# Performance work log

Measured on AMD Instinct MI355X. Metric: run time of the kernel, lower is better.

Reference implementation:

```python
import jax, jax.numpy as jnp
import numpy as np

D_MODEL = 768
NUM_HEADS = 12
D_K = D_MODEL // NUM_HEADS
WINDOW = 16
SPARSITY = 0.8
NEG = -1e9


def _pos_encoding(seq_len, d_model, dtype):
    pos = jnp.arange(seq_len, dtype=jnp.float32)[:, None]
    div = jnp.exp(jnp.arange(0, d_model, 2, dtype=jnp.float32) * (-np.log(10000.0) / d_model))
    pe = jnp.zeros((seq_len, d_model), dtype=jnp.float32)
    pe = pe.at[:, 0::2].set(jnp.sin(pos * div))
    pe = pe.at[:, 1::2].set(jnp.cos(pos * div))
    return pe.astype(dtype)


def _layernorm(x, gamma, beta, eps=1e-5):
    mu = jnp.mean(x, axis=-1, keepdims=True)
    var = jnp.mean(jnp.square(x - mu), axis=-1, keepdims=True)
    return (x - mu) * jax.lax.rsqrt(var + eps) * gamma + beta


def _split_heads(x):  # [B,S,D] -> [B,H,S,dk]
    b, s, _ = x.shape
    return x.reshape(b, s, NUM_HEADS, D_K).transpose(0, 2, 1, 3)


def _attn(q, k, v, mask):  # mask broadcastable to [B,H,S,S], bool
    scores = jnp.einsum('bhqd,bhkd->bhqk', q, k) / jnp.sqrt(jnp.asarray(D_K, q.dtype))
    scores = jnp.where(mask, scores, jnp.asarray(NEG, q.dtype))
    w = jax.nn.softmax(scores, axis=-1)
    out = jnp.einsum('bhqk,bhkd->bhqd', w, v)
    b, h, s, d = out.shape
    return out.transpose(0, 2, 1, 3).reshape(b, s, h * d)


def setup_inputs() -> dict:
    key = jax.random.key(0)
    ks = jax.random.split(key, 16)
    d = D_MODEL
    sc = 1.0 / np.sqrt(d)
    inp = {
        'x': jax.random.normal(ks[0], (2, 2048, d), jnp.float32),
        'wgq': jax.random.normal(ks[1], (d, d), jnp.float32) * sc,
        'wgk': jax.random.normal(ks[2], (d, d), jnp.float32) * sc,
        'wgv': jax.random.normal(ks[3], (d, d), jnp.float32) * sc,
        'wlq': jax.random.normal(ks[4], (d, d), jnp.float32) * sc,
        'wlk': jax.random.normal(ks[5], (d, d), jnp.float32) * sc,
        'wlv': jax.random.normal(ks[6], (d, d), jnp.float32) * sc,
        'wtq': jax.random.normal(ks[7], (d, d), jnp.float32) * sc,
        'wtk': jax.random.normal(ks[8], (d, d), jnp.float32) * sc,
        'wtv': jax.random.normal(ks[9], (d, d), jnp.float32) * sc,
        'w_out': jax.random.normal(ks[10], (3 * d, d), jnp.float32) * (1.0 / np.sqrt(3 * d)),
        'b_out': jnp.zeros((d,), jnp.float32),
        'w_gate': jax.random.normal(ks[11], (d, 3), jnp.float32) * sc,
        'b_gate': jnp.zeros((3,), jnp.float32),
        'w_sparse': jax.random.normal(ks[12], (d, 1), jnp.float32) * sc,
        'b_sparse': jnp.zeros((1,), jnp.float32),
        'g_gamma': jnp.ones((d,), jnp.float32), 'g_beta': jnp.zeros((d,), jnp.float32),
        'l_gamma': jnp.ones((d,), jnp.float32), 'l_beta': jnp.zeros((d,), jnp.float32),
        't_gamma': jnp.ones((d,), jnp.float32), 't_beta': jnp.zeros((d,), jnp.float32),
    }
    return inp


def reference(x, wgq, wgk, wgv, wlq, wlk, wlv, wtq, wtk, wtv,
              w_out, b_out, w_gate, b_gate, w_sparse, b_sparse,
              g_gamma, g_beta, l_gamma, l_beta, t_gamma, t_beta):
    b, s, d = x.shape
    # positional encoding branch input (dropout is identity at eval)
    x_pos = x + _pos_encoding(s, d, x.dtype)[None]

    # focus gate over mean-pooled tokens -> [B,3]
    fw = jax.nn.softmax(x.mean(axis=1) @ w_gate + b_gate, axis=-1)
    gw, lw, tw = fw[:, 0, None, None], fw[:, 1, None, None], fw[:, 2, None, None]

    # sparse (global) mask: keep top-k important columns per batch
    importance = (x @ w_sparse + b_sparse)[..., 0]  # [B,S]
    k = max(1, int((1.0 - SPARSITY) * s))
    _, topk_idx = jax.lax.top_k(importance, k)
    sparse = jnp.zeros((b, s), bool).at[jnp.arange(b)[:, None], topk_idx].set(True)
    sparse_mask = sparse[:, None, None, :]  # [B,1,1,S]

    idx = jnp.arange(s)
    rel = idx[None, :] - idx[:, None]
    half = WINDOW // 2
    local_mask = ((rel >= -half) & (rel <= half))[None, None]  # [1,1,S,S]

    stride = max(1, s // 8)
    temporal_cols = (idx % stride) == 0
    temporal_mask = jnp.broadcast_to(temporal_cols[None, :], (s, s))[None, None]

    # global branch
    g = _attn(_split_heads(x @ wgq), _split_heads(x @ wgk), _split_heads(x @ wgv), sparse_mask)
    g = _layernorm(g, g_gamma, g_beta)
    # local branch
    l = _attn(_split_heads(x @ wlq), _split_heads(x @ wlk), _split_heads(x @ wlv), local_mask)
    l = _layernorm(l, l_gamma, l_beta)
    # temporal branch (uses pos-encoded input)
    t = _attn(_split_heads(x_pos @ wtq), _split_heads(x_pos @ wtk), _split_heads(x_pos @ wtv), temporal_mask)
    t = _layernorm(t, t_gamma, t_beta)

    combined = jnp.concatenate([g * gw, l * lw, t * tw], axis=-1)
    return combined @ w_out + b_out
```

## Files before the change

### kernel.cpp

```cpp
#include <hip/hip_runtime.h>
#include <cstdint>

constexpr int BB   = 2;
constexpr int SS   = 2048;
constexpr int DD   = 768;
constexpr int HH   = 12;
constexpr int NTOK = BB * SS;
constexpr int KSEL = 409;
constexpr int KPAD = 448;
constexpr int NKT  = 7;

typedef __bf16 bf16x8 __attribute__((ext_vector_type(8)));
typedef float  f32x4  __attribute__((ext_vector_type(4)));

__device__ __forceinline__ float b2f(unsigned short u) {
  return __uint_as_float(((unsigned)u) << 16);
}
__device__ __forceinline__ unsigned short f2b(float f) {
  unsigned u = __float_as_uint(f);
  u += 0x7fffu + ((u >> 16) & 1u);
  return (unsigned short)(u >> 16);
}
__device__ __forceinline__ unsigned long long shfl_xor_u64(unsigned long long v, int m) {
  unsigned lo = (unsigned)v, hi = (unsigned)(v >> 32);
  lo = __shfl_xor(lo, m, 64);
  hi = __shfl_xor(hi, m, 64);
  return ((unsigned long long)hi << 32) | lo;
}

__device__ __forceinline__ void gload_lds16(const void* gsrc, void* ldst) {
  __builtin_amdgcn_global_load_lds(
      (__attribute__((address_space(1))) void*)(gsrc),
      (__attribute__((address_space(3))) void*)(ldst), 16, 0, 0);
}

__global__ __launch_bounds__(256) void prep_imp(const float* __restrict__ x,
                                                const float* __restrict__ wsp,
                                                const float* __restrict__ bsp,
                                                unsigned short* __restrict__ xb,
                                                unsigned short* __restrict__ xpb,
                                                float* __restrict__ imp) {
  int srow = blockIdx.x;
  int tid = threadIdx.x;
  const float* xr0 = x + (long)srow * DD;
  const float* xr1 = x + (long)(SS + srow) * DD;
  float acc0 = 0.f, acc1 = 0.f;
#pragma unroll
  for (int k = 0; k < 3; ++k) {
    int c = tid + k * 256;
    int j2 = c & ~1;
    float freq = __expf((float)j2 * -0.011992630692677323f);
    float ang = (float)srow * freq;
    float pe = (c & 1) ? cosf(ang) : sinf(ang);
    float w = wsp[c];
    float x0 = xr0[c], x1 = xr1[c];
    xb[(long)srow * DD + c]        = f2b(x0);
    xb[(long)(SS + srow) * DD + c] = f2b(x1);
    xpb[(long)srow * DD + c]        = f2b(x0 + pe);
    xpb[(long)(SS + srow) * DD + c] = f2b(x1 + pe);
    acc0 += x0 * w;
    acc1 += x1 * w;
  }
#pragma unroll
  for (int m = 1; m < 64; m <<= 1) {
    acc0 += __shfl_xor(acc0, m, 64);
    acc1 += __shfl_xor(acc1, m, 64);
  }
  __shared__ float red[8];
  int wv = tid >> 6, lane = tid & 63;
  if (lane == 0) { red[wv] = acc0; red[4 + wv] = acc1; }
  __syncthreads();
  if (tid == 0) {
    imp[srow]      = red[0] + red[1] + red[2] + red[3] + bsp[0];
    imp[SS + srow] = red[4] + red[5] + red[6] + red[7] + bsp[0];
  }
}

__global__ void transpose_all(const float* w0, const float* w1, const float* w2,
                              const float* w3, const float* w4, const float* w5,
                              const float* w6, const float* w7, const float* w8,
                              const float* w9,
                              unsigned short* WTx4, unsigned short* WTkv,
                              unsigned short* WTqt, unsigned short* WTtkv,
                              unsigned short* WTo) {
  __shared__ float tile[32][33];
  int id = blockIdx.x;
  int z, bx, by;
  if (id < 5184) { z = id / 576; int rem = id % 576; by = rem / 24; bx = rem % 24; }
  else           { z = 9; int rem = id - 5184; by = rem / 24; bx = rem % 24; }
  const float* srcs[10] = {w0, w1, w2, w3, w4, w5, w6, w7, w8, w9};
  const float* src = srcs[z];
  unsigned short* dst;
  int R = DD;
  switch (z) {
    case 0: dst = WTx4;                       break;
    case 1: dst = WTkv;                       break;
    case 2: dst = WTkv + (long)DD * DD;       break;
    case 3: dst = WTx4 + (long)DD * DD;       break;
    case 4: dst = WTx4 + (long)2 * DD * DD;   break;
    case 5: dst = WTx4 + (long)3 * DD * DD;   break;
    case 6: dst = WTqt;                       break;
    case 7: dst = WTtkv;                      break;
    case 8: dst = WTtkv + (long)DD * DD;      break;
    default: dst = WTo; R = 2304;             break;
  }
  int r0 = by * 32;
  int c0 = bx * 32;
  int tx = threadIdx.x, ty = threadIdx.y;
  for (int i = ty; i < 32; i += 8) tile[i][tx] = src[(long)(r0 + i) * DD + c0 + tx];
  __syncthreads();
  for (int i = ty; i < 32; i += 8) dst[(long)(c0 + i) * R + r0 + tx] = f2b(tile[tx][i]);
}

__global__ __launch_bounds__(1024) void topk_kernel(const float* __restrict__ imp,
                                                    int* __restrict__ sel) {
  __shared__ unsigned long long keys[SS];
  int b = blockIdx.x, tid = threadIdx.x;
  for (int i = tid; i < SS; i += 1024) {
    float v = imp[b * SS + i];
    unsigned u = __float_as_uint(v);
    u = (u & 0x80000000u) ? ~u : (u | 0x80000000u);
    unsigned du = ~u;
    keys[i] = ((unsigned long long)du << 32) | (unsigned)i;
  }
  __syncthreads();
  for (int k = 2; k <= SS; k <<= 1) {
    for (int j = k >> 1; j >= 64; j >>= 1) {
      for (int i = tid; i < SS; i += 1024) {
        int p = i ^ j;
        if (p > i) {
          unsigned long long a = keys[i], bb = keys[p];
          bool up = ((i & k) == 0);
          if ((a > bb) == up) { keys[i] = bb; keys[p] = a; }
        }
      }
      __syncthreads();
    }
    unsigned long long k0 = keys[tid], k1 = keys[tid + 1024];
    bool up0 = ((tid & k) == 0);
    bool up1 = (((tid + 1024) & k) == 0);
    int j0 = (k >> 1) < 32 ? (k >> 1) : 32;
    for (int j = j0; j >= 1; j >>= 1) {
      bool low = ((tid & j) == 0);
      unsigned long long p0 = shfl_xor_u64(k0, j);
      k0 = ((low == up0) == (k0 < p0)) ? k0 : p0;
      unsigned long long p1 = shfl_xor_u64(k1, j);
      k1 = ((low == up1) == (k1 < p1)) ? k1 : p1;
    }
    keys[tid] = k0; keys[tid + 1024] = k1;
    __syncthreads();
  }
  for (int i = tid; i < KSEL; i += 1024) sel[b * KSEL + i] = (int)(keys[i] & 0xffffffffu);
}

__global__ __launch_bounds__(256) void gate1(const unsigned short* __restrict__ xb,
                                             float* __restrict__ partial) {
  int b = blockIdx.y, chunk = blockIdx.x, tid = threadIdx.x;
  for (int c = tid; c < DD; c += 256) {
    const unsigned short* xp = xb + ((long)(b * SS + chunk * 128)) * DD + c;
    float acc = 0.f;
    for (int s2 = 0; s2 < 128; ++s2) acc += b2f(xp[(long)s2 * DD]);
    partial[(long)(b * 16 + chunk) * DD + c] = acc;
  }
}

__global__ __launch_bounds__(256) void gate2(const float* __restrict__ partial,
                                             const float* __restrict__ w_gate,
                                             const float* __restrict__ b_gate,
                                             float* __restrict__ fw) {
  int b = blockIdx.x, tid = threadIdx.x;
  __shared__ float meanbuf[DD];
  __shared__ float lg[3];
  for (int c = tid; c < DD; c += 256) {
    float acc = 0.f;
    for (int p = 0; p < 16; ++p) acc += partial[(long)(b * 16 + p) * DD + c];
    meanbuf[c] = acc * (1.0f / (float)SS);
  }
  __syncthreads();
  if (tid < 3) {
    float acc = b_gate[tid];
    for (int d = 0; d < DD; ++d) acc += meanbuf[d] * w_gate[d * 3 + tid];
    lg[tid] = acc;
  }
  __syncthreads();
  if (tid == 0) {
    float mx = fmaxf(lg[0], fmaxf(lg[1], lg[2]));
    float e0 = expf(lg[0] - mx), e1 = expf(lg[1] - mx), e2 = expf(lg[2] - mx);
    float inv = 1.f / (e0 + e1 + e2);
    fw[b * 3 + 0] = e0 * inv; fw[b * 3 + 1] = e1 * inv; fw[b * 3 + 2] = e2 * inv;
  }
}

__global__ __launch_bounds__(192) void gather_pre(const unsigned short* __restrict__ xb,
                                                  const unsigned short* __restrict__ xpb,
                                                  const int* __restrict__ sel,
                                                  unsigned short* __restrict__ A_sel,
                                                  unsigned short* __restrict__ A_t8) {
  int id = blockIdx.x;
  int tid = threadIdx.x;
  if (id < BB * KPAD) {
    int b = id / KPAD, j = id % KPAD;
    uint2* dst = (uint2*)(A_sel + (long)id * DD);
    if (j < KSEL) {
      const uint2* src = (const uint2*)(xb + (long)(b * SS + sel[b * KSEL + j]) * DD);
      dst[tid] = src[tid];
    } else {
      dst[tid] = uint2{0u, 0u};
    }
  } else {
    int r = id - BB * KPAD;
    uint2* dst = (uint2*)(A_t8 + (long)r * DD);
    if (r < 16) {
      int b = r >> 3, j = (r & 7) * 256;
      const uint2* src = (const uint2*)(xpb + (long)(b * SS + j) * DD);
      dst[tid] = src[tid];
    } else {
      dst[tid] = uint2{0u, 0u};
    }
  }
}

__global__ __launch_bounds__(256) void gemm_multi(
    const unsigned short* __restrict__ xb,    const unsigned short* __restrict__ WTx4,
    unsigned short* __restrict__ QKV4,
    const unsigned short* __restrict__ A_sel, const unsigned short* __restrict__ WTkv,
    unsigned short* __restrict__ KVg,
    const unsigned short* __restrict__ xpb,   const unsigned short* __restrict__ WTqt,
    unsigned short* __restrict__ Qt,
    const unsigned short* __restrict__ A_t8,  const unsigned short* __restrict__ WTtkv,
    unsigned short* __restrict__ K8, unsigned short* __restrict__ Vt8,
    unsigned short* __restrict__ Vt, unsigned short* __restrict__ Vtl) {
  __shared__ unsigned short AsB[2][4096];
  __shared__ unsigned short BsB[2][4096];
  constexpr int K = DD;
  const int tid = threadIdx.x;
  const int lane = tid & 63;
  const int wv = tid >> 6;
  const int wr = wv >> 1, wc = wv & 1;

  int lin = blockIdx.x;
  int swz = (lin & 7) * 132 + (lin >> 3);
  const unsigned short *A, *BT;
  int ntx, tile;
  if (swz < 768)       { A = xb;    BT = WTx4;  ntx = 24; tile = swz; }
  else if (swz < 852)  { A = A_sel; BT = WTkv;  ntx = 12; tile = swz - 768; }
  else if (swz < 1044) { A = xpb;   BT = WTqt;  ntx = 6;  tile = swz - 852; }
  else                 { A = A_t8;  BT = WTtkv; ntx = 12; tile = swz - 1044; }
  const long rowBase = (long)(tile / ntx) * 128;
  const long colBase = (long)(tile % ntx) * 128;

  f32x4 acc[4][4];
#pragma unroll
  for (int i = 0; i < 4; ++i)
#pragma unroll
    for (int j = 0; j < 4; ++j)
#pragma unroll
      for (int r = 0; r < 4; ++r) acc[i][j][r] = 0.f;

  const int g0 = tid, g1 = tid + 256;
  const int r0 = g0 >> 2, k80 = (g0 & 3) ^ ((r0 >> 1) & 3);
  const int r1 = g1 >> 2, k81 = (g1 & 3) ^ ((r1 >> 1) & 3);
  const unsigned short* ga0 = A + (rowBase + r0) * (long)K + k80 * 8;
  const unsigned short* ga1 = A + (rowBase + r1) * (long)K + k81 * 8;
  const unsigned short* gb0 = BT + (colBase + r0) * (long)K + k80 * 8;
  const unsigned short* gb1 = BT + (colBase + r1) * (long)K + k81 * 8;

  const int k8 = lane >> 4;
  const int fr = lane & 15;
  int aoff[4], boff[4];
#pragma unroll
  for (int i = 0; i < 4; ++i) {
    int rowA = wr * 64 + i * 16 + fr;
    aoff[i] = (rowA * 4 + (k8 ^ ((rowA >> 1) & 3))) * 8;
    int rowB = wc * 64 + i * 16 + fr;
    boff[i] = (rowB * 4 + (k8 ^ ((rowB >> 1) & 3))) * 8;
  }

  auto stage = [&](int buf, int t) {
    int ko = t * 32;
    gload_lds16(ga0 + ko, &AsB[buf][g0 * 8]);
    gload_lds16(ga1 + ko, &AsB[buf][g1 * 8]);
    gload_lds16(gb0 + ko, &BsB[buf][g0 * 8]);
    gload_lds16(gb1 + ko, &BsB[buf][g1 * 8]);
  };

  constexpr int nk = K >> 5;
  stage(0, 0);
  __syncthreads();
  for (int t = 0; t < nk; ++t) {
    int cur = t & 1;
    if (t + 1 < nk) stage(cur ^ 1, t + 1);
    bf16x8 af[4], bfr[4];
#pragma unroll
    for (int i = 0; i < 4; ++i) af[i] = *(const bf16x8*)(&AsB[cur][aoff[i]]);
#pragma unroll
    for (int i = 0; i < 4; ++i) bfr[i] = *(const bf16x8*)(&BsB[cur][boff[i]]);
#pragma unroll
    for (int mi = 0; mi < 4; ++mi)
#pragma unroll
      for (int ni = 0; ni < 4; ++ni)
        acc[mi][ni] = __builtin_amdgcn_mfma_f32_16x16x32_bf16(af[mi], bfr[ni], acc[mi][ni], 0, 0, 0);
    __syncthreads();
  }

  int mode, vcol0 = 0, N = 0;
  unsigned short* C = nullptr;
  if (swz < 768)       { mode = (colBase >= 2304) ? 1 : 0; C = QKV4; N = 3072;
                         vcol0 = (int)colBase - 2304; }
  else if (swz < 852)  { mode = (colBase >= 768) ? 2 : 0;  C = KVg;  N = 1536;
                         vcol0 = (int)colBase - 768; }
  else if (swz < 1044) { mode = 0; C = Qt; N = 768; }
  else                 { mode = (colBase >= 768) ? 4 : 3;
                         vcol0 = (int)colBase - 768; }

  const int orow0 = (lane >> 4) * 4;
  if (mode == 0) {
#pragma unroll
    for (int mi = 0; mi < 4; ++mi) {
      long gr = rowBase + wr * 64 + mi * 16 + orow0;
#pragma unroll
      for (int ni = 0; ni < 4; ++ni) {
        long gc = colBase + wc * 64 + ni * 16 + fr;
#pragma unroll
        for (int r = 0; r < 4; ++r)
          C[(gr + r) * (long)N + gc] = f2b(acc[mi][ni][r]);
      }
    }
  } else {
#pragma unroll
    for (int mi = 0; mi < 4; ++mi) {
      int lr = wr * 64 + mi * 16 + orow0;
      int grow = (int)rowBase + lr;
#pragma unroll
      for (int ni = 0; ni < 4; ++ni) {
        int lc = wc * 64 + ni * 16 + fr;
        uint2 pk;
        pk.x = (unsigned)f2b(acc[mi][ni][0]) | ((unsigned)f2b(acc[mi][ni][1]) << 16);
        pk.y = (unsigned)f2b(acc[mi][ni][2]) | ((unsigned)f2b(acc[mi][ni][3]) << 16);
        if (mode == 1) {
          int bb2 = grow >> 11, s = grow & (SS - 1);
          *(uint2*)(Vtl + ((long)bb2 * DD + vcol0 + lc) * SS + s) = pk;
        } else if (mode == 2) {
          int bb2 = grow / KPAD, j = grow - bb2 * KPAD;
          *(uint2*)(Vt + ((long)bb2 * DD + vcol0 + lc) * KPAD + j) = pk;
        } else if (mode == 3) {
          if (grow < 16) {
#pragma unroll
            for (int r = 0; r < 4; ++r) {
              int g2 = grow + r;
              K8[((long)(g2 >> 3) * 16 + (g2 & 7)) * DD + colBase + lc] =
                  f2b(acc[mi][ni][r]);
            }
          }
        } else {
          if (grow < 16) {
            *(uint2*)(Vt8 + ((long)(grow >> 3) * DD + vcol0 + lc) * 32 + (grow & 7)) = pk;
          }
        }
      }
    }
    if (mode == 3) {
      int row16 = tid >> 4, cg = tid & 15;
      int bb2 = row16 >> 3, jj = 8 + (row16 & 7);
      uint4 z4 = {0u, 0u, 0u, 0u};
      *(uint4*)(K8 + ((long)bb2 * 16 + jj) * DD + colBase + cg * 8) = z4;
    }
    if (mode == 4) {
#pragma unroll
      for (int e = 0; e < 6; ++e) {
        int id = tid + e * 256;
        int bb2 = id / 768, rem = id % 768;
        int c = rem / 6, ch = rem % 6;
        *(uint2*)(Vt8 + ((long)bb2 * DD + vcol0 + c) * 32 + 8 + ch * 4) = uint2{0u, 0u};
      }
    }
  }
}

__global__ __launch_bounds__(256) void gemm_final_sk(const unsigned short* __restrict__ A,
                                                     const unsigned short* __restrict__ BT,
                                                     float* __restrict__ Cpart) {
  __shared__ unsigned short As[2][128 * 32];
  __shared__ unsigned short Bs[2][128 * 32];
  constexpr int N = 768, K = 2304, CK = 768;
  const int tid = threadIdx.x;
  const int lane = tid & 63;
  const int wv = tid >> 6;
  const int wr = wv >> 1, wc = wv & 1;
  const int z = blockIdx.z;

  int lin = blockIdx.y * gridDim.x + blockIdx.x;
  int swz = (lin & 7) * 24 + (lin >> 3);
  const long rowBase = (long)(swz / 6) * 128;
  const long colBase = (long)(swz % 6) * 128;

  f32x4 acc[4][4];
#pragma unroll
  for (int i = 0; i < 4; ++i)
#pragma unroll
    for (int j = 0; j < 4; ++j)
#pragma unroll
      for (int r = 0; r < 4; ++r) acc[i][j][r] = 0.f;

  const int g0 = tid, g1 = tid + 256;
  const int r0 = g0 >> 2, k80 = (g0 & 3) ^ ((r0 >> 1) & 3);
  const int r1 = g1 >> 2, k81 = (g1 & 3) ^ ((r1 >> 1) & 3);
  const unsigned short* ga0 = A + (rowBase + r0) * (long)K + z * CK + k80 * 8;
  const unsigned short* ga1 = A + (rowBase + r1) * (long)K + z * CK + k81 * 8;
  const unsigned short* gb0 = BT + (colBase + r0) * (long)K + z * CK + k80 * 8;
  const unsigned short* gb1 = BT + (colBase + r1) * (long)K + z * CK + k81 * 8;

  const int k8 = lane >> 4;
  const int fr = lane & 15;
  int aoff[4], boff[4];
#pragma unroll
  for (int i = 0; i < 4; ++i) {
    int rowA = wr * 64 + i * 16 + fr;
    aoff[i] = (rowA * 4 + (k8 ^ ((rowA >> 1) & 3))) * 8;
    int rowB = wc * 64 + i * 16 + fr;
    boff[i] = (rowB * 4 + (k8 ^ ((rowB >> 1) & 3))) * 8;
  }

  auto stage = [&](int buf, int t) {
    int ko = t * 32;
    gload_lds16(ga0 + ko, &As[buf][g0 * 8]);
    gload_lds16(ga1 + ko, &As[buf][g1 * 8]);
    gload_lds16(gb0 + ko, &Bs[buf][g0 * 8]);
    gload_lds16(gb1 + ko, &Bs[buf][g1 * 8]);
  };

  constexpr int nk = CK >> 5;
  stage(0, 0);
  __syncthreads();
  for (int t = 0; t < nk; ++t) {
    int cur = t & 1;
    if (t + 1 < nk) stage(cur ^ 1, t + 1);
    bf16x8 af[4], bfr[4];
#pragma unroll
    for (int i = 0; i < 4; ++i) af[i] = *(const bf16x8*)(&As[cur][aoff[i]]);
#pragma unroll
    for (int i = 0; i < 4; ++i) bfr[i] = *(const bf16x8*)(&Bs[cur][boff[i]]);
#pragma unroll
    for (int mi = 0; mi < 4; ++mi)
#pragma unroll
      for (int ni = 0; ni < 4; ++ni)
        acc[mi][ni] = __builtin_amdgcn_mfma_f32_16x16x32_bf16(af[mi], bfr[ni], acc[mi][ni], 0, 0, 0);
    __syncthreads();
  }

  float* Cz = Cpart + (long)z * NTOK * DD;
  const int orow0 = (lane >> 4) * 4;
#pragma unroll
  for (int mi = 0; mi < 4; ++mi) {
    long gr = rowBase + wr * 64 + mi * 16 + orow0;
#pragma unroll
    for (int ni = 0; ni < 4; ++ni) {
      long gc = colBase + wc * 64 + ni * 16 + fr;
#pragma unroll
      for (int r = 0; r < 4; ++r)
        Cz[(gr + r) * (long)N + gc] = acc[mi][ni][r];
    }
  }
}

__global__ __launch_bounds__(256) void reduce_out(const float* __restrict__ P,
                                                  const float* __restrict__ bias,
                                                  float* __restrict__ out) {
  long i = (long)blockIdx.x * 256 + threadIdx.x;
  const f32x4* p0 = (const f32x4*)P;
  const f32x4* p1 = (const f32x4*)(P + (long)NTOK * DD);
  const f32x4* p2 = (const f32x4*)(P + 2L * NTOK * DD);
  f32x4 v = p0[i];
  v += p1[i];
  v += p2[i];
  int c4 = (int)(i % (DD / 4));
  v += *(const f32x4*)(bias + c4 * 4);
  ((f32x4*)out)[i] = v;
}

__device__ __forceinline__ void attn_flash_body(
    const unsigned short* __restrict__ QKV4,
    const unsigned short* __restrict__ KVg,
    const unsigned short* __restrict__ Vt,
    unsigned short* __restrict__ comb,
    unsigned short* smem) {
  unsigned short* Kl = smem;
  unsigned short* Vl = smem + 8192;
  unsigned short* Pl = smem + 16384;
  int tid = threadIdx.x, w = tid >> 6, lane = tid & 63;
  int fr = lane & 15, g = lane >> 4;
  int b = blockIdx.y / HH, h = blockIdx.y % HH, hoff = h * 64;
  int qbase = blockIdx.x * 64 + w * 16;
  long qrow = (long)b * SS + qbase + fr;

  const unsigned short* qptr = QKV4 + qrow * 3072 + hoff + g * 8;
  bf16x8 bq0 = *(const bf16x8*)(qptr);
  bf16x8 bq1 = *(const bf16x8*)(qptr + 32);

  const int s0 = tid, s1 = tid + 256;
  const int r0 = s0 >> 3, c0 = (s0 & 7) ^ (r0 & 7);
  const int r1 = s1 >> 3, c1 = (s1 & 7) ^ (r1 & 7);
  const unsigned short* kg_b = KVg + (long)b * KPAD * 1536 + hoff;
  const unsigned short* vt_b = Vt + ((long)b * DD + hoff) * KPAD;

  auto stage = [&](int buf, int t0) {
    gload_lds16(kg_b + (long)(t0 * 64 + r0) * 1536 + c0 * 8, &Kl[buf * 4096 + s0 * 8]);
    gload_lds16(kg_b + (long)(t0 * 64 + r1) * 1536 + c1 * 8, &Kl[buf * 4096 + s1 * 8]);
    gload_lds16(vt_b + (long)r0 * KPAD + t0 * 64 + c0 * 8, &Vl[buf * 4096 + s0 * 8]);
    gload_lds16(vt_b + (long)r1 * KPAD + t0 * 64 + c1 * 8, &Vl[buf * 4096 + s1 * 8]);
  };

  f32x4 oacc[4];
#pragma unroll
  for (int mf = 0; mf < 4; ++mf)
#pragma unroll
    for (int r = 0; r < 4; ++r) oacc[mf][r] = 0.f;
  float m = -3.0e38f, l = 0.f;

  stage(0, 0);
  asm volatile("s_waitcnt vmcnt(0)" ::: "memory");
  __syncthreads();

  for (int t = 0; t < NKT; ++t) {
    int cur = t & 1;
    if (t + 1 < NKT) stage(cur ^ 1, t + 1);

    f32x4 st[4];
#pragma unroll
    for (int kt = 0; kt < 4; ++kt) {
      int row = kt * 16 + fr;
      bf16x8 a0 = *(const bf16x8*)(&Kl[cur * 4096 + (row * 8 + (g ^ (row & 7))) * 8]);
      bf16x8 a1 = *(const bf16x8*)(&Kl[cur * 4096 + (row * 8 + ((4 + g) ^ (row & 7))) * 8]);
      f32x4 z = {0.f, 0.f, 0.f, 0.f};
      z = __builtin_amdgcn_mfma_f32_16x16x32_bf16(a0, bq0, z, 0, 0, 0);
      st[kt] = __builtin_amdgcn_mfma_f32_16x16x32_bf16(a1, bq1, z, 0, 0, 0);
    }

    float tm = -3.0e38f;
#pragma unroll
    for (int kt = 0; kt < 4; ++kt)
#pragma unroll
      for (int r = 0; r < 4; ++r) {
        int key = t * 64 + kt * 16 + g * 4 + r;
        float s = (key < KSEL) ? st[kt][r] * 0.125f : -1.0e30f;
        st[kt][r] = s;
        tm = fmaxf(tm, s);
      }
    tm = fmaxf(tm, __shfl_xor(tm, 16, 64));
    tm = fmaxf(tm, __shfl_xor(tm, 32, 64));
    float newm = fmaxf(m, tm);
    float f = __expf(m - newm);
    float tsum = 0.f;
#pragma unroll
    for (int kt = 0; kt < 4; ++kt)
#pragma unroll
      for (int r = 0; r < 4; ++r) {
        float e = __expf(st[kt][r] - newm);
        st[kt][r] = e;
        tsum += e;
      }
    tsum += __shfl_xor(tsum, 16, 64);
    tsum += __shfl_xor(tsum, 32, 64);
    l = l * f + tsum;
    m = newm;
#pragma unroll
    for (int mf = 0; mf < 4; ++mf)
#pragma unroll
      for (int r = 0; r < 4; ++r) oacc[mf][r] *= f;

    unsigned short* pw = &Pl[w * 1088 + fr * 68 + g * 4];
#pragma unroll
    for (int kt = 0; kt < 4; ++kt) {
      uint2 pk;
      pk.x = (unsigned)f2b(st[kt][0]) | ((unsigned)f2b(st[kt][1]) << 16);
      pk.y = (unsigned)f2b(st[kt][2]) | ((unsigned)f2b(st[kt][3]) << 16);
      *(uint2*)(pw + kt * 16) = pk;
    }

    const unsigned short* prd = &Pl[w * 1088 + fr * 68];
#pragma unroll
    for (int ks2 = 0; ks2 < 2; ++ks2) {
      bf16x8 pf = *(const bf16x8*)(prd + ks2 * 32 + g * 8);
#pragma unroll
      for (int mf = 0; mf < 4; ++mf) {
        int vr = mf * 16 + fr;
        int vc = ks2 * 4 + g;
        bf16x8 vf = *(const bf16x8*)(&Vl[cur * 4096 + (vr * 8 + (vc ^ (vr & 7))) * 8]);
        oacc[mf] = __builtin_amdgcn_mfma_f32_16x16x32_bf16(vf, pf, oacc[mf], 0, 0, 0);
      }
    }

    asm volatile("s_waitcnt vmcnt(0)" ::: "memory");
    __syncthreads();
  }

  float inv = 1.f / l;
  unsigned short* orow = comb + qrow * 2304 + hoff;
#pragma unroll
  for (int mf = 0; mf < 4; ++mf) {
    uint2 pk;
    pk.x = (unsigned)f2b(oacc[mf][0] * inv) | ((unsigned)f2b(oacc[mf][1] * inv) << 16);
    pk.y = (unsigned)f2b(oacc[mf][2] * inv) | ((unsigned)f2b(oacc[mf][3] * inv) << 16);
    *(uint2*)(orow + mf * 16 + g * 4) = pk;
  }
}

__device__ __forceinline__ void attn_win_body(
    const unsigned short* __restrict__ QKV,
    const unsigned short* __restrict__ K8,
    const unsigned short* __restrict__ Vt,
    unsigned short* __restrict__ comb, int brOff,
    int LD, int QO, long VSTR, bool local,
    unsigned short* smem) {
  int tid = threadIdx.x, w = tid >> 6, lane = tid & 63;
  int fr = lane & 15, g = lane >> 4;
  int b = blockIdx.y / HH, h = blockIdx.y % HH, hoff = h * 64;
  int qbase = blockIdx.x * 64 + w * 16;
  long qrow = (long)b * SS + qbase + fr;

  const unsigned short* qptr = QKV + qrow * LD + QO + hoff + g * 8;
  bf16x8 bq0 = *(const bf16x8*)(qptr);
  bf16x8 bq1 = *(const bf16x8*)(qptr + 32);

  int kstart = qbase - 8;
  if (kstart < 0) kstart = 0;
  if (kstart > SS - 32) kstart = SS - 32;

  f32x4 st[2];
  if (local) {
#pragma unroll
    for (int kt = 0; kt < 2; ++kt) {
      const unsigned short* kp =
          QKV + ((long)b * SS + kstart + kt * 16 + fr) * LD + 1536 + hoff + g * 8;
      bf16x8 a0 = *(const bf16x8*)(kp);
      bf16x8 a1 = *(const bf16x8*)(kp + 32);
      f32x4 z = {0.f, 0.f, 0.f, 0.f};
      z = __builtin_amdgcn_mfma_f32_16x16x32_bf16(a0, bq0, z, 0, 0, 0);
      st[kt] = __builtin_amdgcn_mfma_f32_16x16x32_bf16(a1, bq1, z, 0, 0, 0);
    }
  } else {
    const unsigned short* kp = K8 + ((long)b * 16 + fr) * DD + hoff + g * 8;
    bf16x8 a0 = *(const bf16x8*)(kp);
    bf16x8 a1 = *(const bf16x8*)(kp + 32);
    f32x4 z = {0.f, 0.f, 0.f, 0.f};
    z = __builtin_amdgcn_mfma_f32_16x16x32_bf16(a0, bq0, z, 0, 0, 0);
    st[0] = __builtin_amdgcn_mfma_f32_16x16x32_bf16(a1, bq1, z, 0, 0, 0);
    st[1] = f32x4{0.f, 0.f, 0.f, 0.f};
  }

  float m = -3.0e38f;
#pragma unroll
  for (int kt = 0; kt < 2; ++kt)
#pragma unroll
    for (int r = 0; r < 4; ++r) {
      int idx = kt * 16 + g * 4 + r;
      bool valid;
      if (local) {
        int rel = kstart + idx - qbase - fr;
        valid = (rel >= -8) && (rel <= 8);
      } else {
        valid = (idx < 8);
      }
      float s = valid ? st[kt][r] * 0.125f : -1.0e30f;
      st[kt][r] = s;
      m = fmaxf(m, s);
    }
  m = fmaxf(m, __shfl_xor(m, 16, 64));
  m = fmaxf(m, __shfl_xor(m, 32, 64));

  float lsum = 0.f;
#pragma unroll
  for (int kt = 0; kt < 2; ++kt)
#pragma unroll
    for (int r = 0; r < 4; ++r) {
      float e = __expf(st[kt][r] - m);
      st[kt][r] = e;
      lsum += e;
    }
  lsum += __shfl_xor(lsum, 16, 64);
  lsum += __shfl_xor(lsum, 32, 64);

  unsigned short* pl = smem + w * 640 + fr * 40 + g * 4;
#pragma unroll
  for (int kt = 0; kt < 2; ++kt) {
    uint2 pk;
    pk.x = (unsigned)f2b(st[kt][0]) | ((unsigned)f2b(st[kt][1]) << 16);
    pk.y = (unsigned)f2b(st[kt][2]) | ((unsigned)f2b(st[kt][3]) << 16);
    *(uint2*)(pl + kt * 16) = pk;
  }

  f32x4 oacc[4];
#pragma unroll
  for (int mf = 0; mf < 4; ++mf)
#pragma unroll
    for (int r = 0; r < 4; ++r) oacc[mf][r] = 0.f;

  const unsigned short* pr = smem + w * 640 + fr * 40 + g * 8;
  bf16x8 pf = *(const bf16x8*)(pr);
  long kb2 = local ? kstart : 0;
#pragma unroll
  for (int mf = 0; mf < 4; ++mf) {
    const unsigned short* vp =
        Vt + ((long)b * DD + hoff + mf * 16 + fr) * VSTR + kb2 + g * 8;
    bf16x8 vf = *(const bf16x8*)(vp);
    oacc[mf] = __builtin_amdgcn_mfma_f32_16x16x32_bf16(vf, pf, oacc[mf], 0, 0, 0);
  }

  float inv = 1.f / lsum;
  unsigned short* orow = comb + qrow * 2304 + brOff + hoff;
#pragma unroll
  for (int mf = 0; mf < 4; ++mf) {
    uint2 pk;
    pk.x = (unsigned)f2b(oacc[mf][0] * inv) | ((unsigned)f2b(oacc[mf][1] * inv) << 16);
    pk.y = (unsigned)f2b(oacc[mf][2] * inv) | ((unsigned)f2b(oacc[mf][3] * inv) << 16);
    *(uint2*)(orow + mf * 16 + g * 4) = pk;
  }
}

__global__ __launch_bounds__(256) void attn_all(
    const unsigned short* __restrict__ QKV4,
    const unsigned short* __restrict__ KVg,
    const unsigned short* __restrict__ Vt,
    const unsigned short* __restrict__ Qt,
    const unsigned short* __restrict__ K8,
    const unsigned short* __restrict__ Vt8,
    const unsigned short* __restrict__ Vtl,
    unsigned short* __restrict__ comb) {
  __shared__ unsigned short smem[20736];
  int z = blockIdx.z;
  if (z == 0) {
    attn_flash_body(QKV4, KVg, Vt, comb, smem);
  } else if (z == 1) {
    attn_win_body(QKV4, nullptr, Vtl, comb, 768, 3072, 768, SS, true, smem);
  } else {
    attn_win_body(Qt, K8, Vt8, comb, 1536, 768, 0, 32, false, smem);
  }
}

__global__ __launch_bounds__(256) void ln_gate_inplace(
    unsigned short* __restrict__ comb,
    const float* __restrict__ gg, const float* __restrict__ gb,
    const float* __restrict__ lgam, const float* __restrict__ lbet,
    const float* __restrict__ tg, const float* __restrict__ tb,
    const float* __restrict__ fw) {
  int row = blockIdx.x;
  int b = row >> 11;
  int tid = threadIdx.x;
  __shared__ float red[8];
  const float* gams[3] = {gg, lgam, tg};
  const float* bets[3] = {gb, lbet, tb};
#pragma unroll
  for (int br = 0; br < 3; ++br) {
    unsigned short* p = comb + (long)row * 2304 + br * DD;
    float x0 = b2f(p[tid]), x1 = b2f(p[tid + 256]), x2 = b2f(p[tid + 512]);
    float s = x0 + x1 + x2;
    float ss = x0 * x0 + x1 * x1 + x2 * x2;
#pragma unroll
    for (int msk = 1; msk < 64; msk <<= 1) {
      s += __shfl_xor(s, msk, 64);
      ss += __shfl_xor(ss, msk, 64);
    }
    int wv = tid >> 6, lane = tid & 63;
    if (lane == 0) { red[wv] = s; red[4 + wv] = ss; }
    __syncthreads();
    float S4 = red[0] + red[1] + red[2] + red[3];
    float SQ = red[4] + red[5] + red[6] + red[7];
    float mean = S4 * (1.f / (float)DD);
    float var = SQ * (1.f / (float)DD) - mean * mean;
    float rs = rsqrtf(var + 1e-5f);
    float gate = fw[b * 3 + br];
    const float* gam = gams[br];
    const float* bet = bets[br];
    p[tid]       = f2b(((x0 - mean) * rs * gam[tid]       + bet[tid])       * gate);
    p[tid + 256] = f2b(((x1 - mean) * rs * gam[tid + 256] + bet[tid + 256]) * gate);
    p[tid + 512] = f2b(((x2 - mean) * rs * gam[tid + 512] + bet[tid + 512]) * gate);
    __syncthreads();
  }
}

extern "C" void kernel_launch(void* const* d_in, const int* in_sizes, int n_in,
                              void* d_out, int out_size, void* d_ws, size_t ws_size,
                              hipStream_t stream) {
  const float* x        = (const float*)d_in[0];
  const float* wgq      = (const float*)d_in[1];
  const float* wgk      = (const float*)d_in[2];
  const float* wgv      = (const float*)d_in[3];
  const float* wlq      = (const float*)d_in[4];
  const float* wlk      = (const float*)d_in[5];
  const float* wlv      = (const float*)d_in[6];
  const float* wtq      = (const float*)d_in[7];
  const float* wtk      = (const float*)d_in[8];
  const float* wtv      = (const float*)d_in[9];
  const float* w_out    = (const float*)d_in[10];
  const float* b_out    = (const float*)d_in[11];
  const float* w_gate   = (const float*)d_in[12];
  const float* b_gate   = (const float*)d_in[13];
  const float* w_sparse = (const float*)d_in[14];
  const float* b_sparse = (const float*)d_in[15];
  const float* g_gamma  = (const float*)d_in[16];
  const float* g_beta   = (const float*)d_in[17];
  const float* l_gamma  = (const float*)d_in[18];
  const float* l_beta   = (const float*)d_in[19];
  const float* t_gamma  = (const float*)d_in[20];
  const float* t_beta   = (const float*)d_in[21];
  float* outp = (float*)d_out;

  unsigned short* xb    = (unsigned short*)d_ws;
  unsigned short* xpb   = xb    + (long)NTOK * DD;
  unsigned short* WTx4  = xpb   + (long)NTOK * DD;
  unsigned short* WTkv  = WTx4  + (long)3072 * DD;
  unsigned short* WTqt  = WTkv  + (long)1536 * DD;
  unsigned short* WTtkv = WTqt  + (long)DD * DD;
  unsigned short* WTo   = WTtkv + (long)1536 * DD;
  unsigned short* QKV4  = WTo   + (long)DD * 2304;
  unsigned short* Qt    = QKV4  + (long)NTOK * 3072;
  unsigned short* A_sel = Qt    + (long)NTOK * DD;
  unsigned short* KVg   = A_sel + (long)BB * KPAD * DD;
  unsigned short* A_t8  = KVg   + (long)BB * KPAD * 1536;
  unsigned short* K8    = A_t8  + (long)128 * DD;
  unsigned short* Vt8   = K8    + (long)BB * 16 * DD;
  unsigned short* Vt    = Vt8   + (long)BB * DD * 32;
  unsigned short* Vtl   = Vt    + (long)BB * DD * KPAD;
  unsigned short* comb  = Vtl   + (long)BB * DD * SS;
  float* Cpart   = (float*)(comb + (long)NTOK * 2304);
  float* imp     = Cpart + 3L * NTOK * DD;
  float* partial = imp + NTOK;
  float* fw      = partial + 32 * DD;
  int*   sel     = (int*)(fw + 8);

  prep_imp<<<SS, 256, 0, stream>>>(x, w_sparse, b_sparse, xb, xpb, imp);
  transpose_all<<<6912, dim3(32, 8), 0, stream>>>(
      wgq, wgk, wgv, wlq, wlk, wlv, wtq, wtk, wtv, w_out,
      WTx4, WTkv, WTqt, WTtkv, WTo);
  topk_kernel<<<BB, 1024, 0, stream>>>(imp, sel);
  gate1<<<dim3(16, BB), 256, 0, stream>>>(xb, partial);
  gate2<<<BB, 256, 0, stream>>>(partial, w_gate, b_gate, fw);

  gather_pre<<<BB * KPAD + 128, 192, 0, stream>>>(xb, xpb, sel, A_sel, A_t8);
  gemm_multi<<<1056, 256, 0, stream>>>(xb, WTx4, QKV4, A_sel, WTkv, KVg,
                                       xpb, WTqt, Qt, A_t8, WTtkv,
                                       K8, Vt8, Vt, Vtl);

  attn_all<<<dim3(32, BB * HH, 3), 256, 0, stream>>>(QKV4, KVg, Vt, Qt, K8, Vt8,
                                                     Vtl, comb);

  ln_gate_inplace<<<NTOK, 256, 0, stream>>>(comb, g_gamma, g_beta,
                                            l_gamma, l_beta, t_gamma, t_beta, fw);
  gemm_final_sk<<<dim3(6, 32, 3), 256, 0, stream>>>(comb, WTo, Cpart);
  reduce_out<<<NTOK * DD / 4 / 256, 256, 0, stream>>>(Cpart, b_out, outp);
}
```

Baseline: 203.5 us.

## Merge preprocessing kernels and gather selected rows inside the GEMM

Folds prep, weight transpose and the gate partial sums into one launch, and merges top-k with gate2 into another, cutting the pre-GEMM launch count from six to two. The gate partial sums now read the fp32 input directly, so they no longer depend on the bf16 copy made in the same launch. The separate gather kernel and its staging buffers are removed: the GEMM computes source row pointers from the selected indices (and the stride-256 rows) when it loads A. This saves a launch and a round trip through memory. The cost is per-row indirection during A loads, and padded rows now read real data instead of zeros, which stays harmless only if those rows are never used downstream.

```diff
diff --git a/kernel.cpp b/kernel.cpp
--- a/kernel.cpp
+++ b/kernel.cpp
@@ -34,188 +34,158 @@
       (__attribute__((address_space(3))) void*)(ldst), 16, 0, 0);
 }
 
-__global__ __launch_bounds__(256) void prep_imp(const float* __restrict__ x,
-                                                const float* __restrict__ wsp,
-                                                const float* __restrict__ bsp,
-                                                unsigned short* __restrict__ xb,
-                                                unsigned short* __restrict__ xpb,
-                                                float* __restrict__ imp) {
-  int srow = blockIdx.x;
-  int tid = threadIdx.x;
-  const float* xr0 = x + (long)srow * DD;
-  const float* xr1 = x + (long)(SS + srow) * DD;
-  float acc0 = 0.f, acc1 = 0.f;
-#pragma unroll
-  for (int k = 0; k < 3; ++k) {
-    int c = tid + k * 256;
-    int j2 = c & ~1;
-    float freq = __expf((float)j2 * -0.011992630692677323f);
-    float ang = (float)srow * freq;
-    float pe = (c & 1) ? cosf(ang) : sinf(ang);
-    float w = wsp[c];
-    float x0 = xr0[c], x1 = xr1[c];
-    xb[(long)srow * DD + c]        = f2b(x0);
-    xb[(long)(SS + srow) * DD + c] = f2b(x1);
-    xpb[(long)srow * DD + c]        = f2b(x0 + pe);
-    xpb[(long)(SS + srow) * DD + c] = f2b(x1 + pe);
-    acc0 += x0 * w;
-    acc1 += x1 * w;
-  }
-#pragma unroll
-  for (int m = 1; m < 64; m <<= 1) {
-    acc0 += __shfl_xor(acc0, m, 64);
-    acc1 += __shfl_xor(acc1, m, 64);
-  }
-  __shared__ float red[8];
-  int wv = tid >> 6, lane = tid & 63;
-  if (lane == 0) { red[wv] = acc0; red[4 + wv] = acc1; }
-  __syncthreads();
-  if (tid == 0) {
-    imp[srow]      = red[0] + red[1] + red[2] + red[3] + bsp[0];
-    imp[SS + srow] = red[4] + red[5] + red[6] + red[7] + bsp[0];
-  }
-}
-
-__global__ void transpose_all(const float* w0, const float* w1, const float* w2,
-                              const float* w3, const float* w4, const float* w5,
-                              const float* w6, const float* w7, const float* w8,
-                              const float* w9,
-                              unsigned short* WTx4, unsigned short* WTkv,
-                              unsigned short* WTqt, unsigned short* WTtkv,
-                              unsigned short* WTo) {
+__global__ __launch_bounds__(256) void mega_pre(
+    const float* __restrict__ x, const float* __restrict__ wsp,
+    const float* __restrict__ bsp,
+    unsigned short* __restrict__ xb, unsigned short* __restrict__ xpb,
+    float* __restrict__ imp,
+    const float* w0, const float* w1, const float* w2, const float* w3,
+    const float* w4, const float* w5, const float* w6, const float* w7,
+    const float* w8, const float* w9,
+    unsigned short* __restrict__ WTx4, unsigned short* __restrict__ WTkv,
+    unsigned short* __restrict__ WTqt, unsigned short* __restrict__ WTtkv,
+    unsigned short* __restrict__ WTo,
+    float* __restrict__ partial) {
   __shared__ float tile[32][33];
   int id = blockIdx.x;
-  int z, bx, by;
-  if (id < 5184) { z = id / 576; int rem = id % 576; by = rem / 24; bx = rem % 24; }
-  else           { z = 9; int rem = id - 5184; by = rem / 24; bx = rem % 24; }
-  const float* srcs[10] = {w0, w1, w2, w3, w4, w5, w6, w7, w8, w9};
-  const float* src = srcs[z];
-  unsigned short* dst;
-  int R = DD;
-  switch (z) {
-    case 0: dst = WTx4;                       break;
-    case 1: dst = WTkv;                       break;
-    case 2: dst = WTkv + (long)DD * DD;       break;
-    case 3: dst = WTx4 + (long)DD * DD;       break;
-    case 4: dst = WTx4 + (long)2 * DD * DD;   break;
-    case 5: dst = WTx4 + (long)3 * DD * DD;   break;
-    case 6: dst = WTqt;                       break;
-    case 7: dst = WTtkv;                      break;
-    case 8: dst = WTtkv + (long)DD * DD;      break;
-    default: dst = WTo; R = 2304;             break;
-  }
-  int r0 = by * 32;
-  int c0 = bx * 32;
-  int tx = threadIdx.x, ty = threadIdx.y;
-  for (int i = ty; i < 32; i += 8) tile[i][tx] = src[(long)(r0 + i) * DD + c0 + tx];
-  __syncthreads();
-  for (int i = ty; i < 32; i += 8) dst[(long)(c0 + i) * R + r0 + tx] = f2b(tile[tx][i]);
-}
-
-__global__ __launch_bounds__(1024) void topk_kernel(const float* __restrict__ imp,
-                                                    int* __restrict__ sel) {
-  __shared__ unsigned long long keys[SS];
-  int b = blockIdx.x, tid = threadIdx.x;
-  for (int i = tid; i < SS; i += 1024) {
-    float v = imp[b * SS + i];
-    unsigned u = __float_as_uint(v);
-    u = (u & 0x80000000u) ? ~u : (u | 0x80000000u);
-    unsigned du = ~u;
-    keys[i] = ((unsigned long long)du << 32) | (unsigned)i;
-  }
-  __syncthreads();
-  for (int k = 2; k <= SS; k <<= 1) {
-    for (int j = k >> 1; j >= 64; j >>= 1) {
-      for (int i = tid; i < SS; i += 1024) {
-        int p = i ^ j;
-        if (p > i) {
-          unsigned long long a = keys[i], bb = keys[p];
-          bool up = ((i & k) == 0);
-          if ((a > bb) == up) { keys[i] = bb; keys[p] = a; }
+  int tid = threadIdx.x;
+
+  if (id < SS) {
+    int srow = id;
+    const float* xr0 = x + (long)srow * DD;
+    const float* xr1 = x + (long)(SS + srow) * DD;
+    float acc0 = 0.f, acc1 = 0.f;
+#pragma unroll
+    for (int k = 0; k < 3; ++k) {
+      int c = tid + k * 256;
+      int j2 = c & ~1;
+      float freq = __expf((float)j2 * -0.011992630692677323f);
+      float ang = (float)srow * freq;
+      float pe = (c & 1) ? cosf(ang) : sinf(ang);
+      float w = wsp[c];
+      float x0 = xr0[c], x1 = xr1[c];
+      xb[(long)srow * DD + c]        = f2b(x0);
+      xb[(long)(SS + srow) * DD + c] = f2b(x1);
+      xpb[(long)srow * DD + c]        = f2b(x0 + pe);
+      xpb[(long)(SS + srow) * DD + c] = f2b(x1 + pe);
+      acc0 += x0 * w;
+      acc1 += x1 * w;
+    }
+#pragma unroll
+    for (int m = 1; m < 64; m <<= 1) {
+      acc0 += __shfl_xor(acc0, m, 64);
+      acc1 += __shfl_xor(acc1, m, 64);
+    }
+    __shared__ float red[8];
+    int wv = tid >> 6, lane = tid & 63;
+    if (lane == 0) { red[wv] = acc0; red[4 + wv] = acc1; }
+    __syncthreads();
+    if (tid == 0) {
+      imp[srow]      = red[0] + red[1] + red[2] + red[3] + bsp[0];
+      imp[SS + srow] = red[4] + red[5] + red[6] + red[7] + bsp[0];
+    }
+  } else if (id < SS + 6912) {
+    int tidx = id - SS;
+    int z, bx, by;
+    if (tidx < 5184) { z = tidx / 576; int rem = tidx % 576; by = rem / 24; bx = rem % 24; }
+    else             { z = 9; int rem = tidx - 5184; by = rem / 24; bx = rem % 24; }
+    const float* srcs[10] = {w0, w1, w2, w3, w4, w5, w6, w7, w8, w9};
+    const float* src = srcs[z];
+    unsigned short* dst;
+    int R = DD;
+    switch (z) {
+      case 0: dst = WTx4;                       break;
+      case 1: dst = WTkv;                       break;
+      case 2: dst = WTkv + (long)DD * DD;       break;
+      case 3: dst = WTx4 + (long)DD * DD;       break;
+      case 4: dst = WTx4 + (long)2 * DD * DD;   break;
+      case 5: dst = WTx4 + (long)3 * DD * DD;   break;
+      case 6: dst = WTqt;                       break;
+      case 7: dst = WTtkv;                      break;
+      case 8: dst = WTtkv + (long)DD * DD;      break;
+      default: dst = WTo; R = 2304;             break;
+    }
+    int r0 = by * 32, c0 = bx * 32;
+    int tx = tid & 31, ty = tid >> 5;
+    for (int i = ty; i < 32; i += 8) tile[i][tx] = src[(long)(r0 + i) * DD + c0 + tx];
+    __syncthreads();
+    for (int i = ty; i < 32; i += 8) dst[(long)(c0 + i) * R + r0 + tx] = f2b(tile[tx][i]);
+  } else {
+    int rem = id - SS - 6912;
+    int chunk = rem & 15, b = rem >> 4;
+    for (int c = tid; c < DD; c += 256) {
+      const float* xp = x + ((long)(b * SS + chunk * 128)) * DD + c;
+      float acc = 0.f;
+      for (int s2 = 0; s2 < 128; ++s2) acc += xp[(long)s2 * DD];
+      partial[(long)(b * 16 + chunk) * DD + c] = acc;
+    }
+  }
+}
+
+__global__ __launch_bounds__(1024) void topk_gate2(
+    const float* __restrict__ imp, int* __restrict__ sel,
+    const float* __restrict__ partial, const float* __restrict__ w_gate,
+    const float* __restrict__ b_gate, float* __restrict__ fw) {
+  int tid = threadIdx.x;
+  if (blockIdx.x < 2) {
+    __shared__ unsigned long long keys[SS];
+    int b = blockIdx.x;
+    for (int i = tid; i < SS; i += 1024) {
+      float v = imp[b * SS + i];
+      unsigned u = __float_as_uint(v);
+      u = (u & 0x80000000u) ? ~u : (u | 0x80000000u);
+      unsigned du = ~u;
+      keys[i] = ((unsigned long long)du << 32) | (unsigned)i;
+    }
+    __syncthreads();
+    for (int k = 2; k <= SS; k <<= 1) {
+      for (int j = k >> 1; j >= 64; j >>= 1) {
+        for (int i = tid; i < SS; i += 1024) {
+          int p = i ^ j;
+          if (p > i) {
+            unsigned long long a = keys[i], bb = keys[p];
+            bool up = ((i & k) == 0);
+            if ((a > bb) == up) { keys[i] = bb; keys[p] = a; }
+          }
         }
+        __syncthreads();
       }
+      unsigned long long k0 = keys[tid], k1 = keys[tid + 1024];
+      bool up0 = ((tid & k) == 0);
+      bool up1 = (((tid + 1024) & k) == 0);
+      int j0 = (k >> 1) < 32 ? (k >> 1) : 32;
+      for (int j = j0; j >= 1; j >>= 1) {
+        bool low = ((tid & j) == 0);
+        unsigned long long p0 = shfl_xor_u64(k0, j);
+        k0 = ((low == up0) == (k0 < p0)) ? k0 : p0;
+        unsigned long long p1 = shfl_xor_u64(k1, j);
+        k1 = ((low == up1) == (k1 < p1)) ? k1 : p1;
+      }
+      keys[tid] = k0; keys[tid + 1024] = k1;
       __syncthreads();
     }
-    unsigned long long k0 = keys[tid], k1 = keys[tid + 1024];
-    bool up0 = ((tid & k) == 0);
-    bool up1 = (((tid + 1024) & k) == 0);
-    int j0 = (k >> 1) < 32 ? (k >> 1) : 32;
-    for (int j = j0; j >= 1; j >>= 1) {
-      bool low = ((tid & j) == 0);
-      unsigned long long p0 = shfl_xor_u64(k0, j);
-      k0 = ((low == up0) == (k0 < p0)) ? k0 : p0;
-      unsigned long long p1 = shfl_xor_u64(k1, j);
-      k1 = ((low == up1) == (k1 < p1)) ? k1 : p1;
-    }
-    keys[tid] = k0; keys[tid + 1024] = k1;
-    __syncthreads();
-  }
-  for (int i = tid; i < KSEL; i += 1024) sel[b * KSEL + i] = (int)(keys[i] & 0xffffffffu);
-}
-
-__global__ __launch_bounds__(256) void gate1(const unsigned short* __restrict__ xb,
-                                             float* __restrict__ partial) {
-  int b = blockIdx.y, chunk = blockIdx.x, tid = threadIdx.x;
-  for (int c = tid; c < DD; c += 256) {
-    const unsigned short* xp = xb + ((long)(b * SS + chunk * 128)) * DD + c;
-    float acc = 0.f;
-    for (int s2 = 0; s2 < 128; ++s2) acc += b2f(xp[(long)s2 * DD]);
-    partial[(long)(b * 16 + chunk) * DD + c] = acc;
-  }
-}
-
-__global__ __launch_bounds__(256) void gate2(const float* __restrict__ partial,
-                                             const float* __restrict__ w_gate,
-                                             const float* __restrict__ b_gate,
-                                             float* __restrict__ fw) {
-  int b = blockIdx.x, tid = threadIdx.x;
-  __shared__ float meanbuf[DD];
-  __shared__ float lg[3];
-  for (int c = tid; c < DD; c += 256) {
-    float acc = 0.f;
-    for (int p = 0; p < 16; ++p) acc += partial[(long)(b * 16 + p) * DD + c];
-    meanbuf[c] = acc * (1.0f / (float)SS);
-  }
-  __syncthreads();
-  if (tid < 3) {
-    float acc = b_gate[tid];
-    for (int d = 0; d < DD; ++d) acc += meanbuf[d] * w_gate[d * 3 + tid];
-    lg[tid] = acc;
-  }
-  __syncthreads();
-  if (tid == 0) {
-    float mx = fmaxf(lg[0], fmaxf(lg[1], lg[2]));
-    float e0 = expf(lg[0] - mx), e1 = expf(lg[1] - mx), e2 = expf(lg[2] - mx);
-    float inv = 1.f / (e0 + e1 + e2);
-    fw[b * 3 + 0] = e0 * inv; fw[b * 3 + 1] = e1 * inv; fw[b * 3 + 2] = e2 * inv;
-  }
-}
-
-__global__ __launch_bounds__(192) void gather_pre(const unsigned short* __restrict__ xb,
-                                                  const unsigned short* __restrict__ xpb,
-                                                  const int* __restrict__ sel,
-                                                  unsigned short* __restrict__ A_sel,
-                                                  unsigned short* __restrict__ A_t8) {
-  int id = blockIdx.x;
-  int tid = threadIdx.x;
-  if (id < BB * KPAD) {
-    int b = id / KPAD, j = id % KPAD;
-    uint2* dst = (uint2*)(A_sel + (long)id * DD);
-    if (j < KSEL) {
-      const uint2* src = (const uint2*)(xb + (long)(b * SS + sel[b * KSEL + j]) * DD);
-      dst[tid] = src[tid];
-    } else {
-      dst[tid] = uint2{0u, 0u};
-    }
+    for (int i = tid; i < KSEL; i += 1024) sel[b * KSEL + i] = (int)(keys[i] & 0xffffffffu);
   } else {
-    int r = id - BB * KPAD;
-    uint2* dst = (uint2*)(A_t8 + (long)r * DD);
-    if (r < 16) {
-      int b = r >> 3, j = (r & 7) * 256;
-      const uint2* src = (const uint2*)(xpb + (long)(b * SS + j) * DD);
-      dst[tid] = src[tid];
-    } else {
-      dst[tid] = uint2{0u, 0u};
+    __shared__ float meanbuf[DD];
+    __shared__ float lg[3];
+    int b = blockIdx.x - 2;
+    if (tid < DD) {
+      float acc = 0.f;
+      for (int p = 0; p < 16; ++p) acc += partial[(long)(b * 16 + p) * DD + tid];
+      meanbuf[tid] = acc * (1.0f / (float)SS);
+    }
+    __syncthreads();
+    if (tid < 3) {
+      float acc = b_gate[tid];
+      for (int d = 0; d < DD; ++d) acc += meanbuf[d] * w_gate[d * 3 + tid];
+      lg[tid] = acc;
+    }
+    __syncthreads();
+    if (tid == 0) {
+      float mx = fmaxf(lg[0], fmaxf(lg[1], lg[2]));
+      float e0 = expf(lg[0] - mx), e1 = expf(lg[1] - mx), e2 = expf(lg[2] - mx);
+      float inv = 1.f / (e0 + e1 + e2);
+      fw[b * 3 + 0] = e0 * inv; fw[b * 3 + 1] = e1 * inv; fw[b * 3 + 2] = e2 * inv;
     }
   }
 }
@@ -223,11 +193,11 @@
 __global__ __launch_bounds__(256) void gemm_multi(
     const unsigned short* __restrict__ xb,    const unsigned short* __restrict__ WTx4,
     unsigned short* __restrict__ QKV4,
-    const unsigned short* __restrict__ A_sel, const unsigned short* __restrict__ WTkv,
-    unsigned short* __restrict__ KVg,
+    const unsigned short* __restrict__ WTkv,  unsigned short* __restrict__ KVg,
     const unsigned short* __restrict__ xpb,   const unsigned short* __restrict__ WTqt,
     unsigned short* __restrict__ Qt,
-    const unsigned short* __restrict__ A_t8,  const unsigned short* __restrict__ WTtkv,
+    const unsigned short* __restrict__ WTtkv,
+    const int* __restrict__ sel,
     unsigned short* __restrict__ K8, unsigned short* __restrict__ Vt8,
     unsigned short* __restrict__ Vt, unsigned short* __restrict__ Vtl) {
   __shared__ unsigned short AsB[2][4096];
@@ -240,14 +210,30 @@
 
   int lin = blockIdx.x;
   int swz = (lin & 7) * 132 + (lin >> 3);
-  const unsigned short *A, *BT;
-  int ntx, tile;
-  if (swz < 768)       { A = xb;    BT = WTx4;  ntx = 24; tile = swz; }
-  else if (swz < 852)  { A = A_sel; BT = WTkv;  ntx = 12; tile = swz - 768; }
-  else if (swz < 1044) { A = xpb;   BT = WTqt;  ntx = 6;  tile = swz - 852; }
-  else                 { A = A_t8;  BT = WTtkv; ntx = 12; tile = swz - 1044; }
+  const unsigned short* BT;
+  int ntx, tile, region;
+  if (swz < 768)       { BT = WTx4;  ntx = 24; tile = swz;        region = 0; }
+  else if (swz < 852)  { BT = WTkv;  ntx = 12; tile = swz - 768;  region = 1; }
+  else if (swz < 1044) { BT = WTqt;  ntx = 6;  tile = swz - 852;  region = 2; }
+  else                 { BT = WTtkv; ntx = 12; tile = swz - 1044; region = 3; }
   const long rowBase = (long)(tile / ntx) * 128;
   const long colBase = (long)(tile % ntx) * 128;
+
+  auto arow = [&](int r) -> const unsigned short* {
+    long grow = rowBase + r;
+    if (region == 0) return xb + grow * (long)K;
+    if (region == 2) return xpb + grow * (long)K;
+    if (region == 1) {
+      int bb2 = (int)(grow / KPAD), j = (int)(grow % KPAD);
+      int srow = (j < KSEL) ? sel[bb2 * KSEL + j] : 0;
+      return xb + ((long)bb2 * SS + srow) * (long)K;
+    }
+    if (grow < 16) {
+      int bb2 = (int)grow >> 3, j = ((int)grow & 7) * 256;
+      return xpb + ((long)bb2 * SS + j) * (long)K;
+    }
+    return xpb;
+  };
 
   f32x4 acc[4][4];
 #pragma unroll
@@ -260,8 +246,8 @@
   const int g0 = tid, g1 = tid + 256;
   const int r0 = g0 >> 2, k80 = (g0 & 3) ^ ((r0 >> 1) & 3);
   const int r1 = g1 >> 2, k81 = (g1 & 3) ^ ((r1 >> 1) & 3);
-  const unsigned short* ga0 = A + (rowBase + r0) * (long)K + k80 * 8;
-  const unsigned short* ga1 = A + (rowBase + r1) * (long)K + k81 * 8;
+  const unsigned short* ga0 = arow(r0) + k80 * 8;
+  const unsigned short* ga1 = arow(r1) + k81 * 8;
   const unsigned short* gb0 = BT + (colBase + r0) * (long)K + k80 * 8;
   const unsigned short* gb1 = BT + (colBase + r1) * (long)K + k81 * 8;
 
@@ -305,13 +291,13 @@
 
   int mode, vcol0 = 0, N = 0;
   unsigned short* C = nullptr;
-  if (swz < 768)       { mode = (colBase >= 2304) ? 1 : 0; C = QKV4; N = 3072;
-                         vcol0 = (int)colBase - 2304; }
-  else if (swz < 852)  { mode = (colBase >= 768) ? 2 : 0;  C = KVg;  N = 1536;
-                         vcol0 = (int)colBase - 768; }
-  else if (swz < 1044) { mode = 0; C = Qt; N = 768; }
-  else                 { mode = (colBase >= 768) ? 4 : 3;
-                         vcol0 = (int)colBase - 768; }
+  if (region == 0)      { mode = (colBase >= 2304) ? 1 : 0; C = QKV4; N = 3072;
+                          vcol0 = (int)colBase - 2304; }
+  else if (region == 1) { mode = (colBase >= 768) ? 2 : 0;  C = KVg;  N = 1536;
+                          vcol0 = (int)colBase - 768; }
+  else if (region == 2) { mode = 0; C = Qt; N = 768; }
+  else                  { mode = (colBase >= 768) ? 4 : 3;
+                          vcol0 = (int)colBase - 768; }
 
   const int orow0 = (lane >> 4) * 4;
   if (mode == 0) {
@@ -814,10 +800,8 @@
   unsigned short* WTo   = WTtkv + (long)1536 * DD;
   unsigned short* QKV4  = WTo   + (long)DD * 2304;
   unsigned short* Qt    = QKV4  + (long)NTOK * 3072;
-  unsigned short* A_sel = Qt    + (long)NTOK * DD;
-  unsigned short* KVg   = A_sel + (long)BB * KPAD * DD;
-  unsigned short* A_t8  = KVg   + (long)BB * KPAD * 1536;
-  unsigned short* K8    = A_t8  + (long)128 * DD;
+  unsigned short* KVg   = Qt    + (long)NTOK * DD;
+  unsigned short* K8    = KVg   + (long)BB * KPAD * 1536;
   unsigned short* Vt8   = K8    + (long)BB * 16 * DD;
   unsigned short* Vt    = Vt8   + (long)BB * DD * 32;
   unsigned short* Vtl   = Vt    + (long)BB * DD * KPAD;
@@ -828,17 +812,14 @@
   float* fw      = partial + 32 * DD;
   int*   sel     = (int*)(fw + 8);
 
-  prep_imp<<<SS, 256, 0, stream>>>(x, w_sparse, b_sparse, xb, xpb, imp);
-  transpose_all<<<6912, dim3(32, 8), 0, stream>>>(
+  mega_pre<<<SS + 6912 + 32, 256, 0, stream>>>(
+      x, w_sparse, b_sparse, xb, xpb, imp,
       wgq, wgk, wgv, wlq, wlk, wlv, wtq, wtk, wtv, w_out,
-      WTx4, WTkv, WTqt, WTtkv, WTo);
-  topk_kernel<<<BB, 1024, 0, stream>>>(imp, sel);
-  gate1<<<dim3(16, BB), 256, 0, stream>>>(xb, partial);
-  gate2<<<BB, 256, 0, stream>>>(partial, w_gate, b_gate, fw);
-
-  gather_pre<<<BB * KPAD + 128, 192, 0, stream>>>(xb, xpb, sel, A_sel, A_t8);
-  gemm_multi<<<1056, 256, 0, stream>>>(xb, WTx4, QKV4, A_sel, WTkv, KVg,
-                                       xpb, WTqt, Qt, A_t8, WTtkv,
+      WTx4, WTkv, WTqt, WTtkv, WTo, partial);
+  topk_gate2<<<4, 1024, 0, stream>>>(imp, sel, partial, w_gate, b_gate, fw);
+
+  gemm_multi<<<1056, 256, 0, stream>>>(xb, WTx4, QKV4, WTkv, KVg,
+                                       xpb, WTqt, Qt, WTtkv, sel,
                                        K8, Vt8, Vt, Vtl);
 
   attn_all<<<dim3(32, BB * HH, 3), 256, 0, stream>>>(QKV4, KVg, Vt, Qt, K8, Vt8,
```

After: 172.0 us. -15.5%, faster.
